# Kernel tuning notes

Hardware: AMD Instinct MI355X
Metric: run time of the kernel (lower is better)

Reference implementation:

```python
import jax, jax.numpy as jnp
import numpy as np

HID = 2048
E = 8          # routed experts
TOP_K = 2
F = 1408       # moe_intermediate_size
FS = 2816      # shared expert intermediate
SCALE = 2.5    # routed_scaling_factor


def setup_inputs() -> dict:
    key = jax.random.key(0)
    ks = jax.random.split(key, 8)
    s = 0.02
    return {
        "hidden_states": jax.random.normal(ks[0], (1, 2048, HID), jnp.float32),
        "w_router": jax.random.normal(ks[1], (HID, E), jnp.float32) * s,
        "w_gate": jax.random.normal(ks[2], (E, HID, F), jnp.float32) * s,
        "w_up": jax.random.normal(ks[3], (E, HID, F), jnp.float32) * s,
        "w_down": jax.random.normal(ks[4], (E, F, HID), jnp.float32) * s,
        "ws_gate": jax.random.normal(ks[5], (HID, FS), jnp.float32) * s,
        "ws_up": jax.random.normal(ks[6], (HID, FS), jnp.float32) * s,
        "ws_down": jax.random.normal(ks[7], (FS, HID), jnp.float32) * s,
    }


def reference(hidden_states, w_router, w_gate, w_up, w_down, ws_gate, ws_up, ws_down):
    B, S, D = hidden_states.shape
    x = hidden_states.reshape(-1, D)                      # [T, D]
    T = x.shape[0]

    # --- router: scores = x @ gate.weight.T (w_router is pre-transposed) ---
    probs = jax.nn.softmax(x @ w_router, axis=-1)         # [T, E]
    top_v, top_i = jax.lax.top_k(probs, TOP_K)            # [T, K]
    top_v = top_v / jnp.sum(top_v, axis=-1, keepdims=True)
    # dense combine weights [T, E] (top-k indices are unique per row)
    combine = jnp.zeros((T, E), x.dtype).at[jnp.arange(T)[:, None], top_i].set(top_v)

    # --- routed experts: SwiGLU MLP per expert, masked combine ---
    g = jax.nn.silu(jnp.einsum("td,edf->etf", x, w_gate))
    u = jnp.einsum("td,edf->etf", x, w_up)
    y = jnp.einsum("etf,efd->etd", g * u, w_down)         # [E, T, D]
    routed = jnp.einsum("etd,te->td", y, combine) * SCALE

    # --- shared experts (always-on SwiGLU MLP) ---
    shared = (jax.nn.silu(x @ ws_gate) * (x @ ws_up)) @ ws_down

    return (routed + shared).reshape(B, S, D)
```

## Files before the change

### kernel.cpp

```cpp
#include <hip/hip_runtime.h>
#include <hip/hip_bf16.h>
#include <stdint.h>

#define TOKS 2048
#define DHID 2048
#define NEXP 8
#define FR 1408
#define FS 2816
#define RSCALE 2.5f

#define G1_SH 352
#define G1_GRID 784
#define G1_Q (G1_GRID / 8)
#define G2_SH 256
#define G2_GRID 880
#define G2_Q (G2_GRID / 8)
#define NIMG_WG 2816
#define NIMG_WD 2816
#define NIMG_SG 704
#define NIMG_SD 704
#define WIMG_GRID (NIMG_WG*2 + NIMG_WD + NIMG_SG*2 + NIMG_SD)

typedef float f32x4 __attribute__((ext_vector_type(4)));
typedef short s16x8 __attribute__((ext_vector_type(8)));

__device__ __forceinline__ ushort f2bf(float f) {
  union { __hip_bfloat16 b; ushort u; } v;
  v.b = __float2bfloat16(f);
  return v.u;
}

__device__ __forceinline__ void gload16(const void* g, void* l) {
  __builtin_amdgcn_global_load_lds(
      (const __attribute__((address_space(1))) unsigned int*)g,
      (__attribute__((address_space(3))) unsigned int*)l, 16, 0, 0);
}

__global__ __launch_bounds__(256) void k_router(
    const float* __restrict__ x, const float* __restrict__ wr,
    ushort* __restrict__ xb, int* __restrict__ top_e, float* __restrict__ top_w) {
  const int wid = threadIdx.x >> 6, lane = threadIdx.x & 63;
  const int t = blockIdx.x * 4 + wid;
  const float* xrow = x + (size_t)t * DHID;
  float acc[NEXP];
#pragma unroll
  for (int e = 0; e < NEXP; ++e) acc[e] = 0.f;
#pragma unroll 4
  for (int j = 0; j < DHID / 64; ++j) {
    const int k = j * 64 + lane;
    const float xv = xrow[k];
    xb[(size_t)t * DHID + k] = f2bf(xv);
    const float4 w0 = *(const float4*)(wr + (size_t)k * 8);
    const float4 w1 = *(const float4*)(wr + (size_t)k * 8 + 4);
    acc[0] += xv * w0.x; acc[1] += xv * w0.y; acc[2] += xv * w0.z; acc[3] += xv * w0.w;
    acc[4] += xv * w1.x; acc[5] += xv * w1.y; acc[6] += xv * w1.z; acc[7] += xv * w1.w;
  }
#pragma unroll
  for (int e = 0; e < NEXP; ++e) {
#pragma unroll
    for (int off = 32; off; off >>= 1) acc[e] += __shfl_xor(acc[e], off);
  }
  if (lane == 0) {
    int i1 = 0;
#pragma unroll
    for (int e = 1; e < NEXP; ++e) if (acc[e] > acc[i1]) i1 = e;
    int i2 = (i1 == 0) ? 1 : 0;
#pragma unroll
    for (int e = 0; e < NEXP; ++e) if (e != i1 && acc[e] > acc[i2]) i2 = e;
    const float w1 = 1.f / (1.f + expf(acc[i2] - acc[i1]));
    top_e[2 * t] = i1; top_e[2 * t + 1] = i2;
    top_w[2 * t] = w1; top_w[2 * t + 1] = 1.f - w1;
  }
}

__global__ __launch_bounds__(256) void k_lists(
    const int* __restrict__ top_e, const float* __restrict__ top_w,
    int* __restrict__ offs, int* __restrict__ ptok, float* __restrict__ pw,
    int* __restrict__ meta, int* __restrict__ mtl) {
  __shared__ int cnt[NEXP], fill[NEXP], loff[NEXP + 1];
  const int tid = threadIdx.x;
  if (tid < NEXP) { cnt[tid] = 0; fill[tid] = 0; }
  __syncthreads();
  for (int p = tid; p < 2 * TOKS; p += 256) atomicAdd(&cnt[top_e[p]], 1);
  __syncthreads();
  if (tid == 0) {
    loff[0] = 0;
    for (int e = 0; e < NEXP; ++e) loff[e + 1] = loff[e] + cnt[e];
    int n = 0;
    for (int e = 0; e < NEXP; ++e)
      for (int m = 0; m * 128 < cnt[e]; ++m) mtl[n++] = (e << 8) | m;
    meta[0] = n;
  }
  __syncthreads();
  for (int p = tid; p < 2 * TOKS; p += 256) {
    const int e = top_e[p];
    const int pos = loff[e] + atomicAdd(&fill[e], 1);
    ptok[pos] = p >> 1;
    pw[pos] = top_w[p];
  }
  if (tid < NEXP + 1) offs[tid] = loff[tid];
}

__global__ __launch_bounds__(256) void k_wimg(
    const float* __restrict__ wg, const float* __restrict__ wu, const float* __restrict__ wd,
    const float* __restrict__ wsg, const float* __restrict__ wsu, const float* __restrict__ wsd,
    ushort* __restrict__ ig, ushort* __restrict__ iu, ushort* __restrict__ id_,
    ushort* __restrict__ isg, ushort* __restrict__ isu, ushort* __restrict__ isd) {
  int id = blockIdx.x;
  const float* src; ushort* dst; int N, ntT, ktT;
  if (id < NIMG_WG)            { src = wg;  dst = ig;  N = FR;   ntT = 11; ktT = 32; }
  else if ((id -= NIMG_WG) < NIMG_WG) { src = wu;  dst = iu;  N = FR;   ntT = 11; ktT = 32; }
  else if ((id -= NIMG_WG) < NIMG_WD) { src = wd;  dst = id_; N = DHID; ntT = 16; ktT = 22; }
  else if ((id -= NIMG_WD) < NIMG_SG) { src = wsg; dst = isg; N = FS;   ntT = 22; ktT = 32; }
  else if ((id -= NIMG_SG) < NIMG_SG) { src = wsu; dst = isu; N = FS;   ntT = 22; ktT = 32; }
  else { id -= NIMG_SG;          src = wsd; dst = isd; N = DHID; ntT = 16; ktT = 44; }
  const int per_e = ntT * ktT;
  const int e = id / per_e, rem = id % per_e;
  const int nt = rem / ktT, kt = rem % ktT;
  const int K = ktT * 64;
  src += (size_t)e * K * N;
  dst += (size_t)id * 8192;

  __shared__ float lds[64][133];
  const int tid = threadIdx.x;
#pragma unroll
  for (int j = 0; j < 8; ++j) {
    const int idx = j * 256 + tid;
    const int row = idx >> 5, c4 = (idx & 31) << 2;
    const float4 v = *(const float4*)(src + (size_t)(kt * 64 + row) * N + nt * 128 + c4);
    lds[row][c4] = v.x; lds[row][c4 + 1] = v.y; lds[row][c4 + 2] = v.z; lds[row][c4 + 3] = v.w;
  }
  __syncthreads();
#pragma unroll
  for (int s = 0; s < 4; ++s) {
    const int sid = s * 256 + tid;
    const int col = sid >> 3, ks = sid & 7;
    ushort tmp[8];
#pragma unroll
    for (int j = 0; j < 8; ++j) tmp[j] = f2bf(lds[ks * 8 + j][col]);
    *(s16x8*)((char*)dst + col * 128 + ((ks ^ (col & 7)) * 16)) = *(const s16x8*)&tmp[0];
  }
}

__global__ __launch_bounds__(256, 2) void k_gemm1i(
    const ushort* __restrict__ xb,
    const ushort* __restrict__ ig, const ushort* __restrict__ iu, ushort* __restrict__ Hr,
    const ushort* __restrict__ isg, const ushort* __restrict__ isu, ushort* __restrict__ Hs,
    const int* __restrict__ offs, const int* __restrict__ ptok,
    const int* __restrict__ meta, const int* __restrict__ mtl) {
  constexpr int KT = DHID / 64;
  const int swz = (blockIdx.x & 7) * G1_Q + (blockIdx.x >> 3);
  int mt, nt, N, base, count;
  const char *imgG, *imgU;
  ushort* H;
  bool gather;
  if (swz < G1_SH) {
    mt = swz & 15; nt = swz >> 4;
    base = 0; count = TOKS; N = FS;
    imgG = (const char*)isg + (size_t)(nt * 32) * 16384;
    imgU = (const char*)isu + (size_t)(nt * 32) * 16384;
    H = Hs; gather = false;
  } else {
    const int r = swz - G1_SH;
    const int n_mt = meta[0];
    if (r >= n_mt * 11) return;
    const int tile = mtl[r / 11];
    nt = r % 11;
    const int e = tile >> 8; mt = tile & 255;
    base = offs[e]; count = offs[e + 1] - base; N = FR;
    imgG = (const char*)ig + (size_t)((e * 11 + nt) * 32) * 16384;
    imgU = (const char*)iu + (size_t)((e * 11 + nt) * 32) * 16384;
    H = Hr; gather = true;
  }

  __shared__ char smem[81920];
  const int tid = threadIdx.x, lane = tid & 63, wid = tid >> 6;
  const int wm = wid >> 1, wn = wid & 1;

  const int aj = tid & 7;
  const ushort* aptr[4];
  uint32_t alds[4];
#pragma unroll
  for (int i = 0; i < 4; ++i) {
    const int row = i * 32 + (tid >> 3);
    const int gr = mt * 128 + row;
    const int arow = gather ? ptok[base + (gr < count ? gr : count - 1)] : gr;
    aptr[i] = xb + (size_t)arow * DHID + aj * 8;
    alds[i] = (uint32_t)(row * 128 + ((aj ^ (row & 7)) * 16));
  }

  const f32x4 fz = {0.f, 0.f, 0.f, 0.f};
  f32x4 accg[4][4], accu[4][4];
#pragma unroll
  for (int mi = 0; mi < 4; ++mi)
#pragma unroll
    for (int ni = 0; ni < 4; ++ni) { accg[mi][ni] = fz; accu[mi][ni] = fz; }

  s16x8 areg[4];
#pragma unroll
  for (int i = 0; i < 4; ++i) areg[i] = *(const s16x8*)(aptr[i]);
#pragma unroll
  for (int i = 0; i < 4; ++i) {
    const int o = (i * 4 + wid) * 1024 + lane * 16;
    gload16(imgG + o, smem + 16384 + o);
    gload16(imgU + o, smem + 32768 + o);
  }

  for (int t = 0; t < KT; ++t) {
    const int bufo = 16384 + (t & 1) * 32768;
#pragma unroll
    for (int i = 0; i < 4; ++i) *(s16x8*)(smem + alds[i]) = areg[i];
    __builtin_amdgcn_sched_barrier(0);
    if (t + 1 < KT) {
#pragma unroll
      for (int i = 0; i < 4; ++i) areg[i] = *(const s16x8*)(aptr[i] + (t + 1) * 64);
      const int nbufo = 16384 + ((t + 1) & 1) * 32768;
      const char* gG = imgG + (size_t)(t + 1) * 16384;
      const char* gU = imgU + (size_t)(t + 1) * 16384;
#pragma unroll
      for (int i = 0; i < 4; ++i) {
        const int o = (i * 4 + wid) * 1024 + lane * 16;
        gload16(gG + o, smem + nbufo + o);
        gload16(gU + o, smem + nbufo + 16384 + o);
      }
      asm volatile("s_waitcnt vmcnt(12) lgkmcnt(0)" ::: "memory");
    } else {
      asm volatile("s_waitcnt vmcnt(0) lgkmcnt(0)" ::: "memory");
    }
    __builtin_amdgcn_sched_barrier(0);
    __builtin_amdgcn_s_barrier();
    __builtin_amdgcn_sched_barrier(0);
#pragma unroll
    for (int kk = 0; kk < 64; kk += 32) {
      s16x8 af[4];
#pragma unroll
      for (int mi = 0; mi < 4; ++mi) {
        const int row = wm * 64 + mi * 16 + (lane & 15);
        const int slot = (kk >> 3) + (lane >> 4);
        af[mi] = *(const s16x8*)(smem + row * 128 + ((slot ^ (row & 7)) * 16));
      }
#pragma unroll
      for (int ni = 0; ni < 4; ++ni) {
        const int colg = wn * 64 + ni * 16 + (lane & 15);
        const int slot = (kk >> 3) + (lane >> 4);
        const uint32_t boff = (uint32_t)(colg * 128 + ((slot ^ (colg & 7)) * 16));
        const s16x8 bg = *(const s16x8*)(smem + bufo + boff);
        const s16x8 bu = *(const s16x8*)(smem + bufo + 16384 + boff);
#pragma unroll
        for (int mi = 0; mi < 4; ++mi) {
          accg[mi][ni] = __builtin_amdgcn_mfma_f32_16x16x32_bf16(af[mi], bg, accg[mi][ni], 0, 0, 0);
          accu[mi][ni] = __builtin_amdgcn_mfma_f32_16x16x32_bf16(af[mi], bu, accu[mi][ni], 0, 0, 0);
        }
      }
    }
    __builtin_amdgcn_s_barrier();
  }

#pragma unroll
  for (int mi = 0; mi < 4; ++mi) {
    const int gr0 = mt * 128 + wm * 64 + mi * 16 + ((lane >> 4) << 2);
#pragma unroll
    for (int ni = 0; ni < 4; ++ni) {
      const int nc = nt * 128 + wn * 64 + ni * 16 + (lane & 15);
#pragma unroll
      for (int r = 0; r < 4; ++r) {
        const int gr = gr0 + r;
        if (gr < count) {
          const float g = accg[mi][ni][r];
          const float u = accu[mi][ni][r];
          const float h = g / (1.f + __expf(-g)) * u;
          H[(size_t)(base + gr) * N + nc] = f2bf(h);
        }
      }
    }
  }
}

__global__ __launch_bounds__(256, 2) void k_gemm2i(
    const ushort* __restrict__ Hr, const ushort* __restrict__ id_,
    const ushort* __restrict__ Hs, const ushort* __restrict__ isd,
    float* __restrict__ out, const int* __restrict__ offs,
    const int* __restrict__ ptok, const float* __restrict__ pw,
    const int* __restrict__ meta, const int* __restrict__ mtl) {
  const int swz = (blockIdx.x & 7) * G2_Q + (blockIdx.x >> 3);
  int mt, nt, base, count, K, KT;
  const ushort* Hbuf;
  const char* img;
  bool routed;
  if (swz < G2_SH) {
    mt = swz & 15; nt = swz >> 4;
    base = 0; count = TOKS; K = FS; KT = 44;
    Hbuf = Hs; img = (const char*)isd + (size_t)(nt * 44) * 16384;
    routed = false;
  } else {
    const int r = swz - G2_SH;
    const int n_mt = meta[0];
    if (r >= n_mt * 16) return;
    const int tile = mtl[r / 16];
    nt = r % 16;
    const int e = tile >> 8; mt = tile & 255;
    base = offs[e]; count = offs[e + 1] - base; K = FR; KT = 22;
    Hbuf = Hr; img = (const char*)id_ + (size_t)((e * 16 + nt) * 22) * 16384;
    routed = true;
  }

  __shared__ char smem[49152];
  const int tid = threadIdx.x, lane = tid & 63, wid = tid >> 6;
  const int wm = wid >> 1, wn = wid & 1;

  const int aj = tid & 7;
  const ushort* aptr[4];
  uint32_t alds[4];
#pragma unroll
  for (int i = 0; i < 4; ++i) {
    const int row = i * 32 + (tid >> 3);
    const int gr = mt * 128 + row;
    const int ar = base + (gr < count ? gr : count - 1);
    aptr[i] = Hbuf + (size_t)ar * K + aj * 8;
    alds[i] = (uint32_t)(row * 128 + ((aj ^ (row & 7)) * 16));
  }

  const f32x4 fz = {0.f, 0.f, 0.f, 0.f};
  f32x4 acc[4][4];
#pragma unroll
  for (int mi = 0; mi < 4; ++mi)
#pragma unroll
    for (int ni = 0; ni < 4; ++ni) acc[mi][ni] = fz;

  s16x8 areg[4];
#pragma unroll
  for (int i = 0; i < 4; ++i) areg[i] = *(const s16x8*)(aptr[i]);
#pragma unroll
  for (int i = 0; i < 4; ++i) {
    const int o = (i * 4 + wid) * 1024 + lane * 16;
    gload16(img + o, smem + 16384 + o);
  }

  for (int t = 0; t < KT; ++t) {
    const int bufo = 16384 + (t & 1) * 16384;
#pragma unroll
    for (int i = 0; i < 4; ++i) *(s16x8*)(smem + alds[i]) = areg[i];
    __builtin_amdgcn_sched_barrier(0);
    if (t + 1 < KT) {
#pragma unroll
      for (int i = 0; i < 4; ++i) areg[i] = *(const s16x8*)(aptr[i] + (t + 1) * 64);
      const int nbufo = 16384 + ((t + 1) & 1) * 16384;
      const char* gB = img + (size_t)(t + 1) * 16384;
#pragma unroll
      for (int i = 0; i < 4; ++i) {
        const int o = (i * 4 + wid) * 1024 + lane * 16;
        gload16(gB + o, smem + nbufo + o);
      }
      asm volatile("s_waitcnt vmcnt(8) lgkmcnt(0)" ::: "memory");
    } else {
      asm volatile("s_waitcnt vmcnt(0) lgkmcnt(0)" ::: "memory");
    }
    __builtin_amdgcn_sched_barrier(0);
    __builtin_amdgcn_s_barrier();
    __builtin_amdgcn_sched_barrier(0);
#pragma unroll
    for (int kk = 0; kk < 64; kk += 32) {
      s16x8 af[4];
#pragma unroll
      for (int mi = 0; mi < 4; ++mi) {
        const int row = wm * 64 + mi * 16 + (lane & 15);
        const int slot = (kk >> 3) + (lane >> 4);
        af[mi] = *(const s16x8*)(smem + row * 128 + ((slot ^ (row & 7)) * 16));
      }
#pragma unroll
      for (int ni = 0; ni < 4; ++ni) {
        const int colg = wn * 64 + ni * 16 + (lane & 15);
        const int slot = (kk >> 3) + (lane >> 4);
        const uint32_t boff = (uint32_t)(colg * 128 + ((slot ^ (colg & 7)) * 16));
        const s16x8 bb = *(const s16x8*)(smem + bufo + boff);
#pragma unroll
        for (int mi = 0; mi < 4; ++mi)
          acc[mi][ni] = __builtin_amdgcn_mfma_f32_16x16x32_bf16(af[mi], bb, acc[mi][ni], 0, 0, 0);
      }
    }
    __builtin_amdgcn_s_barrier();
  }

#pragma unroll
  for (int mi = 0; mi < 4; ++mi) {
    const int gr0 = mt * 128 + wm * 64 + mi * 16 + ((lane >> 4) << 2);
#pragma unroll
    for (int ni = 0; ni < 4; ++ni) {
      const int nc = nt * 128 + wn * 64 + ni * 16 + (lane & 15);
#pragma unroll
      for (int r = 0; r < 4; ++r) {
        const int gr = gr0 + r;
        if (gr < count) {
          const int arow = base + gr;
          const float s = routed ? (RSCALE * pw[arow]) : 1.f;
          const int tok = routed ? ptok[arow] : gr;
          unsafeAtomicAdd(out + (size_t)tok * DHID + nc, acc[mi][ni][r] * s);
        }
      }
    }
  }
}

extern "C" void kernel_launch(void* const* d_in, const int* in_sizes, int n_in,
                              void* d_out, int out_size, void* d_ws, size_t ws_size,
                              hipStream_t stream) {
  const float* x   = (const float*)d_in[0];
  const float* wr  = (const float*)d_in[1];
  const float* wg  = (const float*)d_in[2];
  const float* wu  = (const float*)d_in[3];
  const float* wd  = (const float*)d_in[4];
  const float* wsg = (const float*)d_in[5];
  const float* wsu = (const float*)d_in[6];
  const float* wsd = (const float*)d_in[7];
  float* out = (float*)d_out;

  uint8_t* p = (uint8_t*)d_ws;
  ushort* xb   = (ushort*)p; p += (size_t)TOKS * DHID * 2;
  int* top_e   = (int*)p;    p += (size_t)2 * TOKS * 4;
  float* top_w = (float*)p;  p += (size_t)2 * TOKS * 4;
  int* offs    = (int*)p;    p += 256;
  int* meta    = (int*)p;    p += 64;
  int* mtl     = (int*)p;    p += 256;
  int* ptok    = (int*)p;    p += (size_t)2 * TOKS * 4;
  float* pw    = (float*)p;  p += (size_t)2 * TOKS * 4;
  ushort* Hr   = (ushort*)p; p += (size_t)2 * TOKS * FR * 2;
  ushort* Hs   = (ushort*)p; p += (size_t)TOKS * FS * 2;
  ushort* ig   = (ushort*)p; p += (size_t)NIMG_WG * 8192 * 2;
  ushort* iu   = (ushort*)p; p += (size_t)NIMG_WG * 8192 * 2;
  ushort* id_  = (ushort*)p; p += (size_t)NIMG_WD * 8192 * 2;
  ushort* isg  = (ushort*)p; p += (size_t)NIMG_SG * 8192 * 2;
  ushort* isu  = (ushort*)p; p += (size_t)NIMG_SG * 8192 * 2;
  ushort* isd  = (ushort*)p; p += (size_t)NIMG_SD * 8192 * 2;

  hipMemsetAsync(d_out, 0, (size_t)out_size * sizeof(float), stream);
  k_router<<<TOKS / 4, 256, 0, stream>>>(x, wr, xb, top_e, top_w);
  k_lists<<<1, 256, 0, stream>>>(top_e, top_w, offs, ptok, pw, meta, mtl);
  k_wimg<<<WIMG_GRID, 256, 0, stream>>>(wg, wu, wd, wsg, wsu, wsd,
                                        ig, iu, id_, isg, isu, isd);
  k_gemm1i<<<G1_GRID, 256, 0, stream>>>(xb, ig, iu, Hr, isg, isu, Hs,
                                        offs, ptok, meta, mtl);
  k_gemm2i<<<G2_GRID, 256, 0, stream>>>(Hr, id_, Hs, isd, out,
                                        offs, ptok, pw, meta, mtl);
}
```

Baseline: 385.1 us.

## Widen down-proj GEMM tiles to 256 columns, merge router and weight-image kernels

```diff
diff --git a/kernel.cpp b/kernel.cpp
--- a/kernel.cpp
+++ b/kernel.cpp
@@ -12,14 +12,15 @@
 #define G1_SH 352
 #define G1_GRID 784
 #define G1_Q (G1_GRID / 8)
-#define G2_SH 256
-#define G2_GRID 880
+#define G2_SH 128
+#define G2_GRID 440
 #define G2_Q (G2_GRID / 8)
 #define NIMG_WG 2816
 #define NIMG_WD 2816
 #define NIMG_SG 704
 #define NIMG_SD 704
 #define WIMG_GRID (NIMG_WG*2 + NIMG_WD + NIMG_SG*2 + NIMG_SD)
+#define RW_GRID (512 + WIMG_GRID)
 
 typedef float f32x4 __attribute__((ext_vector_type(4)));
 typedef short s16x8 __attribute__((ext_vector_type(8)));
@@ -36,40 +37,81 @@
       (__attribute__((address_space(3))) unsigned int*)l, 16, 0, 0);
 }
 
-__global__ __launch_bounds__(256) void k_router(
+__global__ __launch_bounds__(256) void k_rwimg(
     const float* __restrict__ x, const float* __restrict__ wr,
-    ushort* __restrict__ xb, int* __restrict__ top_e, float* __restrict__ top_w) {
-  const int wid = threadIdx.x >> 6, lane = threadIdx.x & 63;
-  const int t = blockIdx.x * 4 + wid;
-  const float* xrow = x + (size_t)t * DHID;
-  float acc[NEXP];
-#pragma unroll
-  for (int e = 0; e < NEXP; ++e) acc[e] = 0.f;
+    ushort* __restrict__ xb, int* __restrict__ top_e, float* __restrict__ top_w,
+    const float* __restrict__ wg, const float* __restrict__ wu, const float* __restrict__ wd,
+    const float* __restrict__ wsg, const float* __restrict__ wsu, const float* __restrict__ wsd,
+    ushort* __restrict__ ig, ushort* __restrict__ iu, ushort* __restrict__ id_,
+    ushort* __restrict__ isg, ushort* __restrict__ isu, ushort* __restrict__ isd) {
+  if (blockIdx.x < 512) {
+    const int wid = threadIdx.x >> 6, lane = threadIdx.x & 63;
+    const int t = blockIdx.x * 4 + wid;
+    const float* xrow = x + (size_t)t * DHID;
+    float acc[NEXP];
+#pragma unroll
+    for (int e = 0; e < NEXP; ++e) acc[e] = 0.f;
 #pragma unroll 4
-  for (int j = 0; j < DHID / 64; ++j) {
-    const int k = j * 64 + lane;
-    const float xv = xrow[k];
-    xb[(size_t)t * DHID + k] = f2bf(xv);
-    const float4 w0 = *(const float4*)(wr + (size_t)k * 8);
-    const float4 w1 = *(const float4*)(wr + (size_t)k * 8 + 4);
-    acc[0] += xv * w0.x; acc[1] += xv * w0.y; acc[2] += xv * w0.z; acc[3] += xv * w0.w;
-    acc[4] += xv * w1.x; acc[5] += xv * w1.y; acc[6] += xv * w1.z; acc[7] += xv * w1.w;
-  }
-#pragma unroll
-  for (int e = 0; e < NEXP; ++e) {
-#pragma unroll
-    for (int off = 32; off; off >>= 1) acc[e] += __shfl_xor(acc[e], off);
-  }
-  if (lane == 0) {
-    int i1 = 0;
-#pragma unroll
-    for (int e = 1; e < NEXP; ++e) if (acc[e] > acc[i1]) i1 = e;
-    int i2 = (i1 == 0) ? 1 : 0;
-#pragma unroll
-    for (int e = 0; e < NEXP; ++e) if (e != i1 && acc[e] > acc[i2]) i2 = e;
-    const float w1 = 1.f / (1.f + expf(acc[i2] - acc[i1]));
-    top_e[2 * t] = i1; top_e[2 * t + 1] = i2;
-    top_w[2 * t] = w1; top_w[2 * t + 1] = 1.f - w1;
+    for (int j = 0; j < DHID / 64; ++j) {
+      const int k = j * 64 + lane;
+      const float xv = xrow[k];
+      xb[(size_t)t * DHID + k] = f2bf(xv);
+      const float4 w0 = *(const float4*)(wr + (size_t)k * 8);
+      const float4 w1 = *(const float4*)(wr + (size_t)k * 8 + 4);
+      acc[0] += xv * w0.x; acc[1] += xv * w0.y; acc[2] += xv * w0.z; acc[3] += xv * w0.w;
+      acc[4] += xv * w1.x; acc[5] += xv * w1.y; acc[6] += xv * w1.z; acc[7] += xv * w1.w;
+    }
+#pragma unroll
+    for (int e = 0; e < NEXP; ++e) {
+#pragma unroll
+      for (int off = 32; off; off >>= 1) acc[e] += __shfl_xor(acc[e], off);
+    }
+    if (lane == 0) {
+      int i1 = 0;
+#pragma unroll
+      for (int e = 1; e < NEXP; ++e) if (acc[e] > acc[i1]) i1 = e;
+      int i2 = (i1 == 0) ? 1 : 0;
+#pragma unroll
+      for (int e = 0; e < NEXP; ++e) if (e != i1 && acc[e] > acc[i2]) i2 = e;
+      const float w1 = 1.f / (1.f + expf(acc[i2] - acc[i1]));
+      top_e[2 * t] = i1; top_e[2 * t + 1] = i2;
+      top_w[2 * t] = w1; top_w[2 * t + 1] = 1.f - w1;
+    }
+    return;
+  }
+  int id = blockIdx.x - 512;
+  const float* src; ushort* dst; int N, ntT, ktT;
+  if (id < NIMG_WG)                   { src = wg;  dst = ig;  N = FR;   ntT = 11; ktT = 32; }
+  else if ((id -= NIMG_WG) < NIMG_WG) { src = wu;  dst = iu;  N = FR;   ntT = 11; ktT = 32; }
+  else if ((id -= NIMG_WG) < NIMG_WD) { src = wd;  dst = id_; N = DHID; ntT = 16; ktT = 22; }
+  else if ((id -= NIMG_WD) < NIMG_SG) { src = wsg; dst = isg; N = FS;   ntT = 22; ktT = 32; }
+  else if ((id -= NIMG_SG) < NIMG_SG) { src = wsu; dst = isu; N = FS;   ntT = 22; ktT = 32; }
+  else { id -= NIMG_SG;                 src = wsd; dst = isd; N = DHID; ntT = 16; ktT = 44; }
+  const int per_e = ntT * ktT;
+  const int e = id / per_e, rem = id % per_e;
+  const int nt = rem / ktT, kt = rem % ktT;
+  const int K = ktT * 64;
+  src += (size_t)e * K * N;
+  dst += (size_t)id * 8192;
+
+  __shared__ float lds[64][133];
+  const int tid = threadIdx.x;
+#pragma unroll
+  for (int j = 0; j < 8; ++j) {
+    const int idx = j * 256 + tid;
+    const int row = idx >> 5, c4 = (idx & 31) << 2;
+    const float4 v = *(const float4*)(src + (size_t)(kt * 64 + row) * N + nt * 128 + c4);
+    lds[row][c4] = v.x; lds[row][c4 + 1] = v.y; lds[row][c4 + 2] = v.z; lds[row][c4 + 3] = v.w;
+  }
+  __syncthreads();
+#pragma unroll
+  for (int s = 0; s < 4; ++s) {
+    const int sid = s * 256 + tid;
+    const int col = sid >> 3, ks = sid & 7;
+    ushort tmp[8];
+#pragma unroll
+    for (int j = 0; j < 8; ++j) tmp[j] = f2bf(lds[ks * 8 + j][col]);
+    *(s16x8*)((char*)dst + col * 128 + ((ks ^ (col & 7)) * 16)) = *(const s16x8*)&tmp[0];
   }
 }
 
@@ -99,47 +141,6 @@
     pw[pos] = top_w[p];
   }
   if (tid < NEXP + 1) offs[tid] = loff[tid];
-}
-
-__global__ __launch_bounds__(256) void k_wimg(
-    const float* __restrict__ wg, const float* __restrict__ wu, const float* __restrict__ wd,
-    const float* __restrict__ wsg, const float* __restrict__ wsu, const float* __restrict__ wsd,
-    ushort* __restrict__ ig, ushort* __restrict__ iu, ushort* __restrict__ id_,
-    ushort* __restrict__ isg, ushort* __restrict__ isu, ushort* __restrict__ isd) {
-  int id = blockIdx.x;
-  const float* src; ushort* dst; int N, ntT, ktT;
-  if (id < NIMG_WG)            { src = wg;  dst = ig;  N = FR;   ntT = 11; ktT = 32; }
-  else if ((id -= NIMG_WG) < NIMG_WG) { src = wu;  dst = iu;  N = FR;   ntT = 11; ktT = 32; }
-  else if ((id -= NIMG_WG) < NIMG_WD) { src = wd;  dst = id_; N = DHID; ntT = 16; ktT = 22; }
-  else if ((id -= NIMG_WD) < NIMG_SG) { src = wsg; dst = isg; N = FS;   ntT = 22; ktT = 32; }
-  else if ((id -= NIMG_SG) < NIMG_SG) { src = wsu; dst = isu; N = FS;   ntT = 22; ktT = 32; }
-  else { id -= NIMG_SG;          src = wsd; dst = isd; N = DHID; ntT = 16; ktT = 44; }
-  const int per_e = ntT * ktT;
-  const int e = id / per_e, rem = id % per_e;
-  const int nt = rem / ktT, kt = rem % ktT;
-  const int K = ktT * 64;
-  src += (size_t)e * K * N;
-  dst += (size_t)id * 8192;
-
-  __shared__ float lds[64][133];
-  const int tid = threadIdx.x;
-#pragma unroll
-  for (int j = 0; j < 8; ++j) {
-    const int idx = j * 256 + tid;
-    const int row = idx >> 5, c4 = (idx & 31) << 2;
-    const float4 v = *(const float4*)(src + (size_t)(kt * 64 + row) * N + nt * 128 + c4);
-    lds[row][c4] = v.x; lds[row][c4 + 1] = v.y; lds[row][c4 + 2] = v.z; lds[row][c4 + 3] = v.w;
-  }
-  __syncthreads();
-#pragma unroll
-  for (int s = 0; s < 4; ++s) {
-    const int sid = s * 256 + tid;
-    const int col = sid >> 3, ks = sid & 7;
-    ushort tmp[8];
-#pragma unroll
-    for (int j = 0; j < 8; ++j) tmp[j] = f2bf(lds[ks * 8 + j][col]);
-    *(s16x8*)((char*)dst + col * 128 + ((ks ^ (col & 7)) * 16)) = *(const s16x8*)&tmp[0];
-  }
 }
 
 __global__ __launch_bounds__(256, 2) void k_gemm1i(
@@ -230,6 +231,7 @@
     __builtin_amdgcn_sched_barrier(0);
     __builtin_amdgcn_s_barrier();
     __builtin_amdgcn_sched_barrier(0);
+    __builtin_amdgcn_s_setprio(1);
 #pragma unroll
     for (int kk = 0; kk < 64; kk += 32) {
       s16x8 af[4];
@@ -253,6 +255,7 @@
         }
       }
     }
+    __builtin_amdgcn_s_setprio(0);
     __builtin_amdgcn_s_barrier();
   }
 
@@ -290,21 +293,22 @@
   if (swz < G2_SH) {
     mt = swz & 15; nt = swz >> 4;
     base = 0; count = TOKS; K = FS; KT = 44;
-    Hbuf = Hs; img = (const char*)isd + (size_t)(nt * 44) * 16384;
+    Hbuf = Hs; img = (const char*)isd + (size_t)(2 * nt * 44) * 16384;
     routed = false;
   } else {
     const int r = swz - G2_SH;
     const int n_mt = meta[0];
-    if (r >= n_mt * 16) return;
-    const int tile = mtl[r / 16];
-    nt = r % 16;
+    if (r >= n_mt * 8) return;
+    const int tile = mtl[r >> 3];
+    nt = r & 7;
     const int e = tile >> 8; mt = tile & 255;
     base = offs[e]; count = offs[e + 1] - base; K = FR; KT = 22;
-    Hbuf = Hr; img = (const char*)id_ + (size_t)((e * 16 + nt) * 22) * 16384;
+    Hbuf = Hr; img = (const char*)id_ + (size_t)((e * 16 + 2 * nt) * 22) * 16384;
     routed = true;
   }
-
-  __shared__ char smem[49152];
+  const size_t panstride = (size_t)KT * 16384;
+
+  __shared__ char smem[81920];
   const int tid = threadIdx.x, lane = tid & 63, wid = tid >> 6;
   const int wm = wid >> 1, wn = wid & 1;
 
@@ -321,11 +325,11 @@
   }
 
   const f32x4 fz = {0.f, 0.f, 0.f, 0.f};
-  f32x4 acc[4][4];
+  f32x4 acc[4][8];
 #pragma unroll
   for (int mi = 0; mi < 4; ++mi)
 #pragma unroll
-    for (int ni = 0; ni < 4; ++ni) acc[mi][ni] = fz;
+    for (int ni = 0; ni < 8; ++ni) acc[mi][ni] = fz;
 
   s16x8 areg[4];
 #pragma unroll
@@ -334,30 +338,33 @@
   for (int i = 0; i < 4; ++i) {
     const int o = (i * 4 + wid) * 1024 + lane * 16;
     gload16(img + o, smem + 16384 + o);
+    gload16(img + panstride + o, smem + 32768 + o);
   }
 
   for (int t = 0; t < KT; ++t) {
-    const int bufo = 16384 + (t & 1) * 16384;
+    const int bufo = 16384 + (t & 1) * 32768;
 #pragma unroll
     for (int i = 0; i < 4; ++i) *(s16x8*)(smem + alds[i]) = areg[i];
     __builtin_amdgcn_sched_barrier(0);
     if (t + 1 < KT) {
 #pragma unroll
       for (int i = 0; i < 4; ++i) areg[i] = *(const s16x8*)(aptr[i] + (t + 1) * 64);
-      const int nbufo = 16384 + ((t + 1) & 1) * 16384;
+      const int nbufo = 16384 + ((t + 1) & 1) * 32768;
       const char* gB = img + (size_t)(t + 1) * 16384;
 #pragma unroll
       for (int i = 0; i < 4; ++i) {
         const int o = (i * 4 + wid) * 1024 + lane * 16;
         gload16(gB + o, smem + nbufo + o);
-      }
-      asm volatile("s_waitcnt vmcnt(8) lgkmcnt(0)" ::: "memory");
+        gload16(gB + panstride + o, smem + nbufo + 16384 + o);
+      }
+      asm volatile("s_waitcnt vmcnt(12) lgkmcnt(0)" ::: "memory");
     } else {
       asm volatile("s_waitcnt vmcnt(0) lgkmcnt(0)" ::: "memory");
     }
     __builtin_amdgcn_sched_barrier(0);
     __builtin_amdgcn_s_barrier();
     __builtin_amdgcn_sched_barrier(0);
+    __builtin_amdgcn_s_setprio(1);
 #pragma unroll
     for (int kk = 0; kk < 64; kk += 32) {
       s16x8 af[4];
@@ -368,16 +375,17 @@
         af[mi] = *(const s16x8*)(smem + row * 128 + ((slot ^ (row & 7)) * 16));
       }
 #pragma unroll
-      for (int ni = 0; ni < 4; ++ni) {
-        const int colg = wn * 64 + ni * 16 + (lane & 15);
+      for (int ni = 0; ni < 8; ++ni) {
+        const int c = ni * 16 + (lane & 15);
         const int slot = (kk >> 3) + (lane >> 4);
-        const uint32_t boff = (uint32_t)(colg * 128 + ((slot ^ (colg & 7)) * 16));
+        const uint32_t boff = (uint32_t)(wn * 16384 + c * 128 + ((slot ^ (c & 7)) * 16));
         const s16x8 bb = *(const s16x8*)(smem + bufo + boff);
 #pragma unroll
         for (int mi = 0; mi < 4; ++mi)
           acc[mi][ni] = __builtin_amdgcn_mfma_f32_16x16x32_bf16(af[mi], bb, acc[mi][ni], 0, 0, 0);
       }
     }
+    __builtin_amdgcn_s_setprio(0);
     __builtin_amdgcn_s_barrier();
   }
 
@@ -385,8 +393,8 @@
   for (int mi = 0; mi < 4; ++mi) {
     const int gr0 = mt * 128 + wm * 64 + mi * 16 + ((lane >> 4) << 2);
 #pragma unroll
-    for (int ni = 0; ni < 4; ++ni) {
-      const int nc = nt * 128 + wn * 64 + ni * 16 + (lane & 15);
+    for (int ni = 0; ni < 8; ++ni) {
+      const int nc = nt * 256 + wn * 128 + ni * 16 + (lane & 15);
 #pragma unroll
       for (int r = 0; r < 4; ++r) {
         const int gr = gr0 + r;
@@ -433,10 +441,10 @@
   ushort* isd  = (ushort*)p; p += (size_t)NIMG_SD * 8192 * 2;
 
   hipMemsetAsync(d_out, 0, (size_t)out_size * sizeof(float), stream);
-  k_router<<<TOKS / 4, 256, 0, stream>>>(x, wr, xb, top_e, top_w);
+  k_rwimg<<<RW_GRID, 256, 0, stream>>>(x, wr, xb, top_e, top_w,
+                                       wg, wu, wd, wsg, wsu, wsd,
+                                       ig, iu, id_, isg, isu, isd);
   k_lists<<<1, 256, 0, stream>>>(top_e, top_w, offs, ptok, pw, meta, mtl);
-  k_wimg<<<WIMG_GRID, 256, 0, stream>>>(wg, wu, wd, wsg, wsu, wsd,
-                                        ig, iu, id_, isg, isu, isd);
   k_gemm1i<<<G1_GRID, 256, 0, stream>>>(xb, ig, iu, Hr, isg, isu, Hs,
                                         offs, ptok, meta, mtl);
   k_gemm2i<<<G2_GRID, 256, 0, stream>>>(Hr, id_, Hs, isd, out,
```

After: 389.2 us. No clear change (+1.1%).
